# Kernel optimization log

Hardware: AMD Instinct MI355X
Metric: run time of the kernel (lower is better)

## Reference

```python
import jax, jax.numpy as jnp
import numpy as np
import math

N_HEADS = 16  # matches init_kwargs n_heads


def setup_inputs() -> dict:
    key = jax.random.key(0)
    k1, k2, k3 = jax.random.split(key, 3)
    B, S, D = 8, 1024, 1024
    x = jax.random.normal(k1, (B, S, D), dtype=jnp.float32)
    Wc = jax.random.normal(k2, (D, 3 * D), dtype=jnp.float32) * 0.02
    bc = jnp.zeros((3 * D,), dtype=jnp.float32)
    Wo = jax.random.normal(k3, (D, D), dtype=jnp.float32) * 0.02
    bo = jnp.zeros((D,), dtype=jnp.float32)
    return {"x": x, "Wc": Wc, "bc": bc, "Wo": Wo, "bo": bo}


def reference(x, Wc, bc, Wo, bo):
    B, S, D = x.shape
    H = N_HEADS
    hd = D // H
    qkv = x @ Wc + bc                         # [B,S,3D]
    q, k, v = jnp.split(qkv, 3, axis=2)
    q = q.reshape(B, S, H, hd)
    k = k.reshape(B, S, H, hd)
    v = v.reshape(B, S, H, hd)
    # NOTE: source scales by sqrt(d_size), not sqrt(head_dim)
    scores = jnp.einsum("bqhd,bkhd->bhqk", q, k) / math.sqrt(D)
    # source mask: triu(ones) kept, zeros (k < q) filled with float32 min
    # i.e. attend only to positions k >= q (anti-causal, faithful to source)
    keep = jnp.triu(jnp.ones((S, S), dtype=bool))  # [S,S]
    neg = jnp.finfo(jnp.float32).min
    scores = jnp.where(keep[None, None, :, :], scores, neg)
    attn = jax.nn.softmax(scores, axis=-1)    # [B,H,S,S]; dropout p=0 -> identity
    out = jnp.einsum("bhqk,bkhd->bqhd", attn, v)
    concat = out.reshape(B, S, D)
    return concat @ Wo + bo                   # final dropout p=0 -> identity
```

## Files before the change

kernel.cpp:

```cpp
#include <hip/hip_runtime.h>
#include <stdint.h>

typedef __attribute__((ext_vector_type(8))) short  bf16x8;
typedef __attribute__((ext_vector_type(4))) short  short4v;
typedef __attribute__((ext_vector_type(4))) float  f32x4;
typedef __attribute__((ext_vector_type(4))) float  float4v;

#define VMW(N) asm volatile("s_waitcnt vmcnt(" #N ")" ::: "memory")
#define BAR()  asm volatile("s_barrier" ::: "memory")

__device__ __forceinline__ short f2bf(float f) {
  union { float f; uint32_t u; } c; c.f = f;
  uint32_t u = c.u;
  uint32_t r = (u + 0x7FFFu + ((u >> 16) & 1u)) >> 16;
  return (short)(uint16_t)r;
}

__device__ __forceinline__ void gload_lds16(const void* g, void* l) {
  __builtin_amdgcn_global_load_lds(
      (const __attribute__((address_space(1))) void*)g,
      (__attribute__((address_space(3))) void*)l, 16, 0, 0);
}

__global__ __launch_bounds__(256) void k_f32_to_bf16(
    const float* __restrict__ in, short* __restrict__ out, int n4) {
  int i = blockIdx.x * 256 + threadIdx.x;
  if (i >= n4) return;
  float4v v = *(const float4v*)(in + (size_t)i * 4);
  short4v o;
  o.x = f2bf(v.x); o.y = f2bf(v.y); o.z = f2bf(v.z); o.w = f2bf(v.w);
  *(short4v*)(out + (size_t)i * 4) = o;
}

__global__ __launch_bounds__(256) void k_transpose_bf16(
    const float* __restrict__ in, short* __restrict__ out, int R, int C) {
  __shared__ short tile[64][65];
  int bc = blockIdx.x * 64, br = blockIdx.y * 64;
  int tc = threadIdx.x & 63, tr = threadIdx.x >> 6;
#pragma unroll
  for (int i = 0; i < 64; i += 4)
    tile[tc][tr + i] = f2bf(in[(size_t)(br + tr + i) * C + bc + tc]);
  __syncthreads();
#pragma unroll
  for (int i = 0; i < 64; i += 4)
    out[(size_t)(bc + tr + i) * R + br + tc] = tile[tr + i][tc];
}

template <bool F32OUT>
__global__ __launch_bounds__(256) void k_gemm2(
    const short* __restrict__ A, const short* __restrict__ BT,
    const float* __restrict__ bias, void* __restrict__ Cout,
    int M, int N, int K, int nbn) {
  __shared__ short SM[2][2][2][128][32];
  const int tid = threadIdx.x;
  const int w = tid >> 6, l = tid & 63;
  const int fr = l & 15, fg = l >> 4;
  const int wm = w >> 1, wn = w & 1;

  const int q8 = gridDim.x >> 3;
  const int wg = (blockIdx.x & 7) * q8 + (blockIdx.x >> 3);
  const int bm = wg / nbn, bn = wg % nbn;
  const size_t brow = (size_t)bm << 7;
  const int bcol = bn << 7;

  const int NT = K >> 6;

  const int srow = l >> 2;
  const int soct = (l & 3) ^ ((l >> 3) & 3);
  const short* aG = A + (brow + srow) * (size_t)K + soct * 8;
  const short* bG = BT + ((size_t)(bcol + srow)) * K + soct * 8;

  const int slot8 = ((fg ^ ((fr >> 1) & 3)) << 3);

  f32x4 acc[4][4] = {};

#pragma unroll
  for (int s = 0; s < 6; ++s) {
    const int t = s >> 2, tau = s & 3, buf = t & 1, mat = tau & 1, kh = tau >> 1;
    const int kbase = t * 64 + kh * 32;
    const short* g0 = (mat ? bG : aG) + kbase;
#pragma unroll
    for (int j = 0; j < 2; ++j) {
      const int r0 = (w * 2 + j) * 16;
      gload_lds16(g0 + (size_t)r0 * K, (char*)&SM[buf][mat][kh][r0][0]);
    }
  }
  VMW(8);
  BAR();

  int sidx = 6;
  for (int t = 0; t < NT; ++t) {
    const int buf = t & 1;
#pragma unroll
    for (int p = 0; p < 4; ++p) {
      const int mh = p & 1, kh = p >> 1;
      bf16x8 af[2], bf[4];
#pragma unroll
      for (int m = 0; m < 2; ++m)
        af[m] = *(const bf16x8*)
            &SM[buf][0][kh][wm * 64 + mh * 32 + m * 16 + fr][slot8];
#pragma unroll
      for (int n = 0; n < 4; ++n)
        bf[n] = *(const bf16x8*)&SM[buf][1][kh][wn * 64 + n * 16 + fr][slot8];
      if (sidx < NT * 4) {
        const int ts = sidx >> 2, tau = sidx & 3;
        const int sb = ts & 1, mat = tau & 1, skh = tau >> 1;
        const int kbase = ts * 64 + skh * 32;
        const short* g0 = (mat ? bG : aG) + kbase;
#pragma unroll
        for (int j = 0; j < 2; ++j) {
          const int r0 = (w * 2 + j) * 16;
          gload_lds16(g0 + (size_t)r0 * K, (char*)&SM[sb][mat][skh][r0][0]);
        }
        ++sidx;
      }
      BAR();
      __builtin_amdgcn_s_setprio(1);
#pragma unroll
      for (int m = 0; m < 2; ++m)
#pragma unroll
        for (int n = 0; n < 4; ++n)
          acc[mh * 2 + m][n] = __builtin_amdgcn_mfma_f32_16x16x32_bf16(
              af[m], bf[n], acc[mh * 2 + m][n], 0, 0, 0);
      __builtin_amdgcn_s_setprio(0);
      if (p == 1) {
        if (t == NT - 1) { VMW(0); } else { VMW(8); }
      } else if (p == 3 && t < NT - 1) {
        if (t == NT - 2) { VMW(4); } else { VMW(8); }
      }
      BAR();
    }
  }

#pragma unroll
  for (int n = 0; n < 4; ++n) {
    const int col = bcol + wn * 64 + n * 16 + fr;
    const float bv = bias[col];
#pragma unroll
    for (int i = 0; i < 4; ++i) {
      const size_t row = brow + (size_t)(wm * 64 + i * 16 + fg * 4);
#pragma unroll
      for (int r = 0; r < 4; ++r) {
        const float v = acc[i][n][r] + bv;
        if (F32OUT)
          ((float*)Cout)[(row + r) * (size_t)N + col] = v;
        else
          ((short*)Cout)[(row + r) * (size_t)N + col] = f2bf(v);
      }
    }
  }
}

__global__ __launch_bounds__(256) void k_attn(
    const short* __restrict__ qkv, short* __restrict__ outc, int Bn, int S) {
  __shared__ short Ks[128][64];
  __shared__ short Vt[64][136];

  const int tid = threadIdx.x;
  const int w = tid >> 6, l = tid & 63;
  const int fr = l & 15, fg = l >> 4;

  const int tq = blockIdx.x >> 7;
  const int bh = blockIdx.x & 127;
  const int h = bh & 15, b = bh >> 4;
  const int q0 = tq << 6;

  const size_t rowbase = (size_t)b * S;
  const int qcol = q0 + w * 16 + fr;

  bf16x8 qf[2];
  {
    const short* qp = qkv + (rowbase + qcol) * 3072 + h * 64 + fg * 8;
    qf[0] = *(const bf16x8*)qp;
    qf[1] = *(const bf16x8*)(qp + 32);
  }

  f32x4 o[4] = {};
  float m2 = -3.0e38f, ls = 0.0f;

  const short* Kbase = qkv + rowbase * 3072 + 1024 + h * 64;
  const short* Vbase = qkv + rowbase * 3072 + 2048 + h * 64;
  const float C2 = 0.04508422f;

  const int c0 = tq >> 1;
  for (int c = c0; c < 8; ++c) {
    const int k0 = c << 7;
    {
      int r8 = l >> 3, slot = l & 7;
#pragma unroll
      for (int j = 0; j < 4; ++j) {
        int ch = w * 4 + j;
        int row = ch * 8 + r8;
        int d = (slot ^ (row & 7)) << 3;
        gload_lds16(Kbase + (size_t)(k0 + row) * 3072 + d,
                    (char*)&Ks[0][0] + ch * 1024);
      }
    }
    {
      int db = (tid >> 4) << 2;
#pragma unroll
      for (int kh = 0; kh < 2; ++kh) {
        int kb = ((tid & 15) << 2) + (kh << 6);
        const short* vp = Vbase + (size_t)(k0 + kb) * 3072 + db;
        short4v r0 = *(const short4v*)(vp);
        short4v r1 = *(const short4v*)(vp + 3072);
        short4v r2 = *(const short4v*)(vp + 2 * 3072);
        short4v r3 = *(const short4v*)(vp + 3 * 3072);
        short4v t0 = {r0.x, r1.x, r2.x, r3.x};
        short4v t1 = {r0.y, r1.y, r2.y, r3.y};
        short4v t2 = {r0.z, r1.z, r2.z, r3.z};
        short4v t3 = {r0.w, r1.w, r2.w, r3.w};
        *(short4v*)&Vt[db + 0][kb] = t0;
        *(short4v*)&Vt[db + 1][kb] = t1;
        *(short4v*)&Vt[db + 2][kb] = t2;
        *(short4v*)&Vt[db + 3][kb] = t3;
      }
    }
    __syncthreads();

    f32x4 st[8];
#pragma unroll
    for (int kb = 0; kb < 8; ++kb) {
      f32x4 z = {0.f, 0.f, 0.f, 0.f};
      int row = kb * 16 + fr;
      int sw = row & 7;
      bf16x8 kf0 = *(const bf16x8*)&Ks[row][(fg ^ sw) << 3];
      bf16x8 kf1 = *(const bf16x8*)&Ks[row][((4 + fg) ^ sw) << 3];
      z = __builtin_amdgcn_mfma_f32_16x16x32_bf16(kf0, qf[0], z, 0, 0, 0);
      z = __builtin_amdgcn_mfma_f32_16x16x32_bf16(kf1, qf[1], z, 0, 0, 0);
      st[kb] = z;
    }

    const bool masked = (c == c0);
    float pm = -3.0e38f;
#pragma unroll
    for (int kb = 0; kb < 8; ++kb)
#pragma unroll
      for (int r = 0; r < 4; ++r) {
        float s = st[kb][r] * C2;
        if (masked) {
          int kg = k0 + kb * 16 + fg * 4 + r;
          s = (kg < qcol) ? -3.0e38f : s;
        }
        st[kb][r] = s;
        pm = fmaxf(pm, s);
      }
    pm = fmaxf(pm, __shfl_xor(pm, 16, 64));
    pm = fmaxf(pm, __shfl_xor(pm, 32, 64));

    bool skip = __all(pm - m2 <= 8.0f);
    float mnew = skip ? m2 : fmaxf(m2, pm);
    float psum = 0.f;
#pragma unroll
    for (int kb = 0; kb < 8; ++kb)
#pragma unroll
      for (int r = 0; r < 4; ++r) {
        float e = exp2f(st[kb][r] - mnew);
        st[kb][r] = e;
        psum += e;
      }
    psum += __shfl_xor(psum, 16, 64);
    psum += __shfl_xor(psum, 32, 64);
    if (skip) {
      ls += psum;
    } else {
      float scl = exp2f(m2 - mnew);
      ls = ls * scl + psum;
      m2 = mnew;
#pragma unroll
      for (int r = 0; r < 4; ++r) {
        float so = __shfl(scl, fg * 4 + r, 64);
#pragma unroll
        for (int f = 0; f < 4; ++f) o[f][r] *= so;
      }
    }

#pragma unroll
    for (int kb2 = 0; kb2 < 4; ++kb2) {
      bf16x8 pa = {f2bf(st[2 * kb2][0]),     f2bf(st[2 * kb2][1]),
                   f2bf(st[2 * kb2][2]),     f2bf(st[2 * kb2][3]),
                   f2bf(st[2 * kb2 + 1][0]), f2bf(st[2 * kb2 + 1][1]),
                   f2bf(st[2 * kb2 + 1][2]), f2bf(st[2 * kb2 + 1][3])};
#pragma unroll
      for (int f = 0; f < 4; ++f) {
        short4v v0 = *(const short4v*)&Vt[f * 16 + fr][kb2 * 32 + fg * 4];
        short4v v1 = *(const short4v*)&Vt[f * 16 + fr][kb2 * 32 + 16 + fg * 4];
        bf16x8 vb = {v0.x, v0.y, v0.z, v0.w, v1.x, v1.y, v1.z, v1.w};
        o[f] = __builtin_amdgcn_mfma_f32_16x16x32_bf16(pa, vb, o[f], 0, 0, 0);
      }
    }
    __syncthreads();
  }

#pragma unroll
  for (int r = 0; r < 4; ++r) {
    float denom = __shfl(ls, fg * 4 + r, 64);
    float inv = 1.0f / denom;
    size_t orow = rowbase + (size_t)(q0 + w * 16 + fg * 4 + r);
    short* op = outc + orow * 1024 + h * 64 + fr;
#pragma unroll
    for (int f = 0; f < 4; ++f) op[f * 16] = f2bf(o[f][r] * inv);
  }
}

extern "C" void kernel_launch(void* const* d_in, const int* in_sizes, int n_in,
                              void* d_out, int out_size, void* d_ws,
                              size_t ws_size, hipStream_t stream) {
  const float* x = (const float*)d_in[0];
  const float* Wc = (const float*)d_in[1];
  const float* bc = (const float*)d_in[2];
  const float* Wo = (const float*)d_in[3];
  const float* bo = (const float*)d_in[4];
  float* out = (float*)d_out;

  const int Bn = 8, S = 1024, D = 1024;
  const int M = Bn * S;

  char* ws = (char*)d_ws;
  short* xb  = (short*)(ws);
  short* wct = (short*)(ws + (size_t)16 * 1024 * 1024);
  short* wot = (short*)(ws + (size_t)22 * 1024 * 1024);
  short* qkv = (short*)(ws + (size_t)24 * 1024 * 1024);
  short* cat = (short*)(ws + (size_t)72 * 1024 * 1024);

  k_f32_to_bf16<<<(M * D / 4 + 255) / 256, 256, 0, stream>>>(x, xb, M * D / 4);
  {
    dim3 g(3 * D / 64, D / 64);
    k_transpose_bf16<<<g, 256, 0, stream>>>(Wc, wct, D, 3 * D);
  }
  {
    dim3 g(D / 64, D / 64);
    k_transpose_bf16<<<g, 256, 0, stream>>>(Wo, wot, D, D);
  }
  k_gemm2<false><<<(M / 128) * (3 * D / 128), 256, 0, stream>>>(
      xb, wct, bc, qkv, M, 3 * D, D, 3 * D / 128);
  k_attn<<<16 * 128, 256, 0, stream>>>(qkv, cat, Bn, S);
  k_gemm2<true><<<(M / 128) * (D / 128), 256, 0, stream>>>(
      cat, wot, bo, out, M, D, D, D / 128);
}
```

Baseline: 174.7 us.

## Replace 128x128 GEMM with 256x256-tile, 512-thread kernel with full-K64 double buffering

Both projection GEMMs now use a new kernel with 256x256 output tiles, 8 waves, and 64-wide K slices double-buffered in LDS, using an XOR swizzle. Each wave computes a 128x64 sub-tile and loads its B fragments once per K step. The goal is higher arithmetic intensity and fewer global loads per FLOP. In exchange it uses more LDS and registers, and launches far fewer workgroups: the output GEMM drops to 128 blocks, which may underfill the 256 CUs. It also waits on vmcnt(0) every iteration, which weakens load/compute overlap.

```diff
diff --git a/kernel.cpp b/kernel.cpp
--- a/kernel.cpp
+++ b/kernel.cpp
@@ -7,6 +7,7 @@
 typedef __attribute__((ext_vector_type(4))) float  float4v;
 
 #define VMW(N) asm volatile("s_waitcnt vmcnt(" #N ")" ::: "memory")
+#define LKW(N) asm volatile("s_waitcnt lgkmcnt(" #N ")" ::: "memory")
 #define BAR()  asm volatile("s_barrier" ::: "memory")
 
 __device__ __forceinline__ short f2bf(float f) {
@@ -47,101 +48,107 @@
 }
 
 template <bool F32OUT>
-__global__ __launch_bounds__(256) void k_gemm2(
+__global__ __launch_bounds__(512) void k_g256(
     const short* __restrict__ A, const short* __restrict__ BT,
     const float* __restrict__ bias, void* __restrict__ Cout,
     int M, int N, int K, int nbn) {
-  __shared__ short SM[2][2][2][128][32];
+  __shared__ short As[2][2][128][64];
+  __shared__ short Bs[2][2][128][64];
   const int tid = threadIdx.x;
   const int w = tid >> 6, l = tid & 63;
   const int fr = l & 15, fg = l >> 4;
-  const int wm = w >> 1, wn = w & 1;
+  const int wm = w >> 2, wn = w & 3;
 
   const int q8 = gridDim.x >> 3;
   const int wg = (blockIdx.x & 7) * q8 + (blockIdx.x >> 3);
   const int bm = wg / nbn, bn = wg % nbn;
-  const size_t brow = (size_t)bm << 7;
-  const int bcol = bn << 7;
-
+  const size_t brow = (size_t)bm << 8;
+  const int bcol = bn << 8;
   const int NT = K >> 6;
 
-  const int srow = l >> 2;
-  const int soct = (l & 3) ^ ((l >> 3) & 3);
-  const short* aG = A + (brow + srow) * (size_t)K + soct * 8;
-  const short* bG = BT + ((size_t)(bcol + srow)) * K + soct * 8;
-
-  const int slot8 = ((fg ^ ((fr >> 1) & 3)) << 3);
-
-  f32x4 acc[4][4] = {};
-
-#pragma unroll
-  for (int s = 0; s < 6; ++s) {
-    const int t = s >> 2, tau = s & 3, buf = t & 1, mat = tau & 1, kh = tau >> 1;
-    const int kbase = t * 64 + kh * 32;
-    const short* g0 = (mat ? bG : aG) + kbase;
-#pragma unroll
-    for (int j = 0; j < 2; ++j) {
-      const int r0 = (w * 2 + j) * 16;
-      gload_lds16(g0 + (size_t)r0 * K, (char*)&SM[buf][mat][kh][r0][0]);
-    }
-  }
-  VMW(8);
+  const int srow = tid >> 3;
+  const int soct = (tid & 7) ^ (srow & 7);
+  const int sx = fr & 7;
+
+  f32x4 acc[8][4] = {};
+
+#define STAGE_A(bufv, halfv, kt)                                               \
+  {                                                                            \
+    _Pragma("unroll") for (int j = 0; j < 2; ++j) {                            \
+      const short* g = A + (brow + (halfv)*128 + j * 64 + srow) * (size_t)K +  \
+                       (kt)*64 + soct * 8;                                     \
+      gload_lds16(g, (char*)&As[bufv][halfv][j * 64 + w * 8][0]);              \
+    }                                                                          \
+  }
+#define STAGE_B(bufv, halfv, kt)                                               \
+  {                                                                            \
+    _Pragma("unroll") for (int j = 0; j < 2; ++j) {                            \
+      const short* g = BT +                                                    \
+                       ((size_t)(bcol + (halfv)*128 + j * 64 + srow)) * K +    \
+                       (kt)*64 + soct * 8;                                     \
+      gload_lds16(g, (char*)&Bs[bufv][halfv][j * 64 + w * 8][0]);              \
+    }                                                                          \
+  }
+
+  STAGE_A(0, 0, 0); STAGE_B(0, 0, 0); STAGE_A(0, 1, 0); STAGE_B(0, 1, 0);
+  VMW(0);
   BAR();
 
-  int sidx = 6;
+  const int bhalf = wn >> 1, brow2 = (wn & 1) * 64;
+
   for (int t = 0; t < NT; ++t) {
-    const int buf = t & 1;
+    const int buf = t & 1, nbuf = buf ^ 1;
+    bf16x8 bfr[4][2];
 #pragma unroll
     for (int p = 0; p < 4; ++p) {
-      const int mh = p & 1, kh = p >> 1;
-      bf16x8 af[2], bf[4];
-#pragma unroll
-      for (int m = 0; m < 2; ++m)
-        af[m] = *(const bf16x8*)
-            &SM[buf][0][kh][wm * 64 + mh * 32 + m * 16 + fr][slot8];
-#pragma unroll
-      for (int n = 0; n < 4; ++n)
-        bf[n] = *(const bf16x8*)&SM[buf][1][kh][wn * 64 + n * 16 + fr][slot8];
-      if (sidx < NT * 4) {
-        const int ts = sidx >> 2, tau = sidx & 3;
-        const int sb = ts & 1, mat = tau & 1, skh = tau >> 1;
-        const int kbase = ts * 64 + skh * 32;
-        const short* g0 = (mat ? bG : aG) + kbase;
-#pragma unroll
-        for (int j = 0; j < 2; ++j) {
-          const int r0 = (w * 2 + j) * 16;
-          gload_lds16(g0 + (size_t)r0 * K, (char*)&SM[sb][mat][skh][r0][0]);
-        }
-        ++sidx;
-      }
+      bf16x8 afr[2][2];
+#pragma unroll
+      for (int i = 0; i < 2; ++i)
+#pragma unroll
+        for (int kk = 0; kk < 2; ++kk)
+          afr[i][kk] = *(const bf16x8*)
+              &As[buf][wm][(2 * p + i) * 16 + fr][((kk * 4 + fg) ^ sx) * 8];
+      if (p == 0) {
+#pragma unroll
+        for (int nf = 0; nf < 4; ++nf)
+#pragma unroll
+          for (int kk = 0; kk < 2; ++kk)
+            bfr[nf][kk] = *(const bf16x8*)
+                &Bs[buf][bhalf][brow2 + nf * 16 + fr][((kk * 4 + fg) ^ sx) * 8];
+      }
+      if (t + 1 < NT) {
+        if (p == 0) { STAGE_A(nbuf, 0, t + 1); STAGE_B(nbuf, 0, t + 1); }
+        else if (p == 1) { STAGE_A(nbuf, 1, t + 1); STAGE_B(nbuf, 1, t + 1); }
+      }
+      if (p == 0) { LKW(8); }
       BAR();
       __builtin_amdgcn_s_setprio(1);
 #pragma unroll
-      for (int m = 0; m < 2; ++m)
-#pragma unroll
-        for (int n = 0; n < 4; ++n)
-          acc[mh * 2 + m][n] = __builtin_amdgcn_mfma_f32_16x16x32_bf16(
-              af[m], bf[n], acc[mh * 2 + m][n], 0, 0, 0);
+      for (int i = 0; i < 2; ++i)
+#pragma unroll
+        for (int nf = 0; nf < 4; ++nf)
+#pragma unroll
+          for (int kk = 0; kk < 2; ++kk)
+            acc[2 * p + i][nf] = __builtin_amdgcn_mfma_f32_16x16x32_bf16(
+                afr[i][kk], bfr[nf][kk], acc[2 * p + i][nf], 0, 0, 0);
       __builtin_amdgcn_s_setprio(0);
-      if (p == 1) {
-        if (t == NT - 1) { VMW(0); } else { VMW(8); }
-      } else if (p == 3 && t < NT - 1) {
-        if (t == NT - 2) { VMW(4); } else { VMW(8); }
-      }
+      if (p == 3 && t + 1 < NT) { VMW(0); }
       BAR();
     }
   }
-
-#pragma unroll
-  for (int n = 0; n < 4; ++n) {
-    const int col = bcol + wn * 64 + n * 16 + fr;
+#undef STAGE_A
+#undef STAGE_B
+
+#pragma unroll
+  for (int nf = 0; nf < 4; ++nf) {
+    const int col = bcol + wn * 64 + nf * 16 + fr;
     const float bv = bias[col];
 #pragma unroll
-    for (int i = 0; i < 4; ++i) {
-      const size_t row = brow + (size_t)(wm * 64 + i * 16 + fg * 4);
+    for (int mf = 0; mf < 8; ++mf) {
+      const size_t row = brow + (size_t)(wm * 128 + mf * 16 + fg * 4);
 #pragma unroll
       for (int r = 0; r < 4; ++r) {
-        const float v = acc[i][n][r] + bv;
+        const float v = acc[mf][nf][r] + bv;
         if (F32OUT)
           ((float*)Cout)[(row + r) * (size_t)N + col] = v;
         else
@@ -332,9 +339,9 @@
     dim3 g(D / 64, D / 64);
     k_transpose_bf16<<<g, 256, 0, stream>>>(Wo, wot, D, D);
   }
-  k_gemm2<false><<<(M / 128) * (3 * D / 128), 256, 0, stream>>>(
-      xb, wct, bc, qkv, M, 3 * D, D, 3 * D / 128);
+  k_g256<false><<<(M / 256) * (3 * D / 256), 512, 0, stream>>>(
+      xb, wct, bc, qkv, M, 3 * D, D, 3 * D / 256);
   k_attn<<<16 * 128, 256, 0, stream>>>(qkv, cat, Bn, S);
-  k_gemm2<true><<<(M / 128) * (D / 128), 256, 0, stream>>>(
-      cat, wot, bo, out, M, D, D, D / 128);
-}
+  k_g256<true><<<(M / 256) * (D / 256), 512, 0, stream>>>(
+      cat, wot, bo, out, M, D, D, D / 256);
+}
```

Measured after the change: 190.5 us. +9.0%, slower.
